# Kernel tuning notes

Hardware: AMD Instinct MI355X
Metric: run time of the kernel (lower is better)

Reference implementation:

```python
import jax, jax.numpy as jnp
import numpy as np

N = 100000   # num_nodes
E = 1600000  # num_edges
IN, HID, OUT = 128, 128, 64
BN_EPS = 1e-5


def setup_inputs() -> dict:
    key = jax.random.key(0)
    ks = jax.random.split(key, 8)
    x = jax.random.normal(ks[0], (N, IN), jnp.float32)
    edge_index = jax.random.randint(ks[1], (2, E), 0, N)
    edge_weight = jax.random.uniform(ks[2], (E,), jnp.float32)
    W1 = jax.random.normal(ks[3], (IN, HID), jnp.float32) / np.sqrt(IN)
    b1 = jnp.zeros((HID,), jnp.float32)
    gamma = jnp.ones((HID,), jnp.float32)
    beta = jnp.zeros((HID,), jnp.float32)
    W2 = jax.random.normal(ks[4], (HID, OUT), jnp.float32) / np.sqrt(HID)
    b2 = jnp.zeros((OUT,), jnp.float32)
    return {"x": x, "edge_index": edge_index, "edge_weight": edge_weight,
            "W1": W1, "b1": b1, "gamma": gamma, "beta": beta, "W2": W2, "b2": b2}


def _add_self_loops(edge_index, edge_weight, n):
    loops = jnp.arange(n, dtype=edge_index.dtype)
    row = jnp.concatenate([edge_index[0], loops])
    col = jnp.concatenate([edge_index[1], loops])
    ew = jnp.concatenate([edge_weight, jnp.ones((n,), edge_weight.dtype)])
    return row, col, ew


def _gcn_conv(x, row, col, ew, W, b, n):
    h = x @ W                                           # [n, out]
    deg = jax.ops.segment_sum(ew, col, num_segments=n)  # in-degree (incl. self-loops)
    dinv = jnp.where(deg > 0, jax.lax.rsqrt(jnp.where(deg > 0, deg, 1.0)), 0.0)
    norm = dinv[row] * ew * dinv[col]                   # [E+n]
    msg = h[row] * norm[:, None]                        # gather + scale
    out = jax.ops.segment_sum(msg, col, num_segments=n)  # scatter-add at targets
    return out + b


def reference(x, edge_index, edge_weight, W1, b1, gamma, beta, W2, b2):
    n = x.shape[0]
    row, col, ew = _add_self_loops(edge_index, edge_weight, n)
    h = _gcn_conv(x, row, col, ew, W1, b1, n)
    # BatchNorm1d over nodes (training-mode batch stats, biased variance)
    mu = h.mean(axis=0)
    var = ((h - mu) ** 2).mean(axis=0)
    h = (h - mu) * jax.lax.rsqrt(var + BN_EPS) * gamma + beta
    h = jax.nn.relu(h)
    # dropout is identity at inference
    h = _gcn_conv(h, row, col, ew, W2, b2, n)
    return jax.nn.log_softmax(h, axis=1)  # out_feats > 1 branch
```

## Files before the change

kernel.cpp:

```cpp
#include <hip/hip_runtime.h>
#include <math.h>


typedef unsigned int   uint;
typedef unsigned short ushort;
typedef __bf16 bf16x8 __attribute__((ext_vector_type(8)));
typedef float  f32x4  __attribute__((ext_vector_type(4)));

#define EPB  4096
#define BSH  9

union U16 { uint4 u; bf16x8 b; };

__device__ __forceinline__ void atomAddF(float* p, float v) {
    __hip_atomic_fetch_add(p, v, __ATOMIC_RELAXED, __HIP_MEMORY_SCOPE_AGENT);
}

__device__ __forceinline__ ushort f2bf(float f) {
    uint u = __float_as_uint(f);
    u += 0x7FFFu + ((u >> 16) & 1u);
    return (ushort)(u >> 16);
}
__device__ __forceinline__ float bf2f(ushort h) {
    return __uint_as_float(((uint)h) << 16);
}
__device__ __forceinline__ uint pack2(float f0, float f1) {
    return (uint)f2bf(f0) | ((uint)f2bf(f1) << 16);
}
__device__ __forceinline__ void fma8(float* acc, uint4 v, float w) {
    acc[0] = fmaf(bf2f((ushort)(v.x)),       w, acc[0]);
    acc[1] = fmaf(bf2f((ushort)(v.x >> 16)), w, acc[1]);
    acc[2] = fmaf(bf2f((ushort)(v.y)),       w, acc[2]);
    acc[3] = fmaf(bf2f((ushort)(v.y >> 16)), w, acc[3]);
    acc[4] = fmaf(bf2f((ushort)(v.z)),       w, acc[4]);
    acc[5] = fmaf(bf2f((ushort)(v.z >> 16)), w, acc[5]);
    acc[6] = fmaf(bf2f((ushort)(v.w)),       w, acc[6]);
    acc[7] = fmaf(bf2f((ushort)(v.w >> 16)), w, acc[7]);
}

__global__ __launch_bounds__(256)
void k_p1(const int* __restrict__ col, int* __restrict__ ghist,
          int e, int PB) {
    __shared__ int lh[256];
    lh[threadIdx.x] = 0;
    __syncthreads();
    int base = blockIdx.x * EPB;
    int end  = base + EPB; if (end > e) end = e;
    for (int j = base + threadIdx.x; j < end; j += 256)
        atomicAdd(&lh[col[j] >> BSH], 1);
    __syncthreads();
    ghist[threadIdx.x * PB + blockIdx.x] = lh[threadIdx.x];
}

__global__ __launch_bounds__(256)
void k_scanA(const int* __restrict__ v, int* __restrict__ bsum, int tot) {
    __shared__ int ls[256];
    int base = blockIdx.x * 1024 + threadIdx.x * 4;
    int s = 0;
#pragma unroll
    for (int k = 0; k < 4; ++k) { int i = base + k; if (i < tot) s += v[i]; }
    ls[threadIdx.x] = s;
    __syncthreads();
    for (int d = 128; d > 0; d >>= 1) {
        if (threadIdx.x < d) ls[threadIdx.x] += ls[threadIdx.x + d];
        __syncthreads();
    }
    if (threadIdx.x == 0) bsum[blockIdx.x] = ls[0];
}

__global__ __launch_bounds__(1024)
void k_scanB(int* __restrict__ bsum, float* __restrict__ bn, int nblk) {
    __shared__ int ls[1024];
    int t = threadIdx.x;
    if (t < 256) bn[t] = 0.0f;
    int v = (t < nblk) ? bsum[t] : 0;
    ls[t] = v;
    __syncthreads();
    for (int d = 1; d < 1024; d <<= 1) {
        int mine = ls[t];
        int up   = (t >= d) ? ls[t - d] : 0;
        __syncthreads();
        ls[t] = mine + up;
        __syncthreads();
    }
    if (t < nblk) bsum[t] = ls[t] - v;
}

__global__ __launch_bounds__(256)
void k_scanC(const int* __restrict__ v, const int* __restrict__ bsum,
             int* __restrict__ gout, int tot) {
    __shared__ int ls[256];
    int base = blockIdx.x * 1024 + threadIdx.x * 4;
    int w[4];
#pragma unroll
    for (int k = 0; k < 4; ++k) { int i = base + k; w[k] = (i < tot) ? v[i] : 0; }
    int t = w[0] + w[1] + w[2] + w[3];
    ls[threadIdx.x] = t;
    __syncthreads();
    for (int d = 1; d < 256; d <<= 1) {
        int mine = ls[threadIdx.x];
        int up   = (threadIdx.x >= d) ? ls[threadIdx.x - d] : 0;
        __syncthreads();
        ls[threadIdx.x] = mine + up;
        __syncthreads();
    }
    int off = bsum[blockIdx.x] + ls[threadIdx.x] - t;
    int pf = 0;
#pragma unroll
    for (int k = 0; k < 4; ++k) {
        int i = base + k;
        if (i < tot) gout[i] = off + pf;
        pf += w[k];
    }
}

__global__ __launch_bounds__(256)
void k_p3(const int* __restrict__ row, const int* __restrict__ col,
          const float* __restrict__ ew, const int* __restrict__ goff,
          int2* __restrict__ ebuf, int e, int PB) {
    __shared__ int cur[256];
    cur[threadIdx.x] = 0;
    __syncthreads();
    int blk  = blockIdx.x;
    int base = blk * EPB;
    int end  = base + EPB; if (end > e) end = e;
    for (int j = base + threadIdx.x; j < end; j += 256) {
        int c = col[j];
        int b = c >> BSH;
        int r = atomicAdd(&cur[b], 1);
        int pos = goff[b * PB + blk] + r;
        ebuf[pos] = make_int2(row[j] | ((c & ((1 << BSH) - 1)) << 17),
                              __float_as_int(ew[j]));
    }
}

__global__ __launch_bounds__(512)
void k_p4a(const int* __restrict__ goff, const int2* __restrict__ ebuf,
           int* __restrict__ ptr, float* __restrict__ dinv,
           int n, int e, int PB, int NB) {
    __shared__ int   cnt[512];
    __shared__ float fs[512];
    __shared__ int   sc[512];
    int tid = threadIdx.x;
    int b   = blockIdx.x;
    int bstart = goff[b * PB];
    int bend   = (b == NB - 1) ? e : goff[(b + 1) * PB];

    cnt[tid] = 0; fs[tid] = 0.f;
    __syncthreads();

    for (int j = bstart + tid; j < bend; j += 512) {
        int2 eb = ebuf[j];
        int c = (eb.x >> 17) & 511;
        atomicAdd(&cnt[c], 1);
        atomicAdd(&fs[c], __int_as_float(eb.y));
    }
    __syncthreads();

    int v = cnt[tid];
    sc[tid] = v;
    __syncthreads();
    for (int d = 1; d < 512; d <<= 1) {
        int mine = sc[tid];
        int up   = (tid >= d) ? sc[tid - d] : 0;
        __syncthreads();
        sc[tid] = mine + up;
        __syncthreads();
    }
    int excl = sc[tid] - v;

    int node = (b << BSH) + tid;
    if (node < n) {
        ptr[node]  = bstart + excl;
        dinv[node] = rsqrtf(1.0f + fs[tid]);
    }
    if (b == 0 && tid == 0) ptr[n] = e;
}

__global__ __launch_bounds__(512)
void k_p4b(const int* __restrict__ goff, const int2* __restrict__ ebuf,
           const int* __restrict__ ptr, const float* __restrict__ dinv,
           int2* __restrict__ csr, int n, int e, int PB, int NB) {
    __shared__ int   cur[512];
    __shared__ float dl[512];
    int tid = threadIdx.x;
    int b   = blockIdx.x;
    int bstart = goff[b * PB];
    int bend   = (b == NB - 1) ? e : goff[(b + 1) * PB];

    cur[tid] = 0;
    int node = (b << BSH) + tid;
    dl[tid] = (node < n) ? dinv[node] : 0.f;
    __syncthreads();

    for (int j = bstart + tid; j < bend; j += 512) {
        int2 eb = ebuf[j];
        int c   = (eb.x >> 17) & 511;
        int src = eb.x & 0x1FFFF;
        int r = atomicAdd(&cur[c], 1);
        float w = __int_as_float(eb.y) * dinv[src] * dl[c];
        csr[ptr[(b << BSH) + c] + r] = make_int2(src, __float_as_int(w));
    }
}

__global__ void k_wfrag(const float* __restrict__ W, uint4* __restrict__ Wf, int M) {
    int t = blockIdx.x * 256 + threadIdx.x;
    if (t >= M * 16) return;
    int l  = t & 63;
    int ks = (t >> 6) & 3;
    int nt = t >> 8;
    int kbase = ks * 32 + (l >> 4) * 8;
    int colj  = nt * 16 + (l & 15);
    float v[8];
#pragma unroll
    for (int j = 0; j < 8; ++j) v[j] = W[(kbase + j) * M + colj];
    uint4 o;
    o.x = pack2(v[0], v[1]);
    o.y = pack2(v[2], v[3]);
    o.z = pack2(v[4], v[5]);
    o.w = pack2(v[6], v[7]);
    Wf[t] = o;
}

template<int M, bool BN>
__global__ __launch_bounds__(256)
void k_mfma(const void* __restrict__ Xv, const uint4* __restrict__ Wf,
            const float* __restrict__ scale, const float* __restrict__ shift,
            ushort* __restrict__ H, int n)
{
    constexpr int NT = M / 16;
    const int l = threadIdx.x & 63;
    const int w = threadIdx.x >> 6;
    const int rowbase = blockIdx.x * 64 + w * 16;
    const int arow = rowbase + (l & 15);
    const bool rv = arow < n;
    const int koff = (l >> 4) * 8;

    f32x4 acc[NT];
#pragma unroll
    for (int t = 0; t < NT; ++t) acc[t] = (f32x4){0.f, 0.f, 0.f, 0.f};

#pragma unroll
    for (int ks = 0; ks < 4; ++ks) {
        U16 ua;
        if (BN) {
            const ushort* xr = (const ushort*)Xv + (size_t)arow * 128 + koff;
            U16 xa; xa.u = make_uint4(0, 0, 0, 0);
            if (rv) xa.u = *(const uint4*)(xr + ks * 32);
            int k0 = ks * 32 + koff;
            float4 sc0 = *(const float4*)(scale + k0);
            float4 sc1 = *(const float4*)(scale + k0 + 4);
            float4 sh0 = *(const float4*)(shift + k0);
            float4 sh1 = *(const float4*)(shift + k0 + 4);
            float a[8];
            a[0] = fmaxf(0.f, fmaf(bf2f((ushort)(xa.u.x)),       sc0.x, sh0.x));
            a[1] = fmaxf(0.f, fmaf(bf2f((ushort)(xa.u.x >> 16)), sc0.y, sh0.y));
            a[2] = fmaxf(0.f, fmaf(bf2f((ushort)(xa.u.y)),       sc0.z, sh0.z));
            a[3] = fmaxf(0.f, fmaf(bf2f((ushort)(xa.u.y >> 16)), sc0.w, sh0.w));
            a[4] = fmaxf(0.f, fmaf(bf2f((ushort)(xa.u.z)),       sc1.x, sh1.x));
            a[5] = fmaxf(0.f, fmaf(bf2f((ushort)(xa.u.z >> 16)), sc1.y, sh1.y));
            a[6] = fmaxf(0.f, fmaf(bf2f((ushort)(xa.u.w)),       sc1.z, sh1.z));
            a[7] = fmaxf(0.f, fmaf(bf2f((ushort)(xa.u.w >> 16)), sc1.w, sh1.w));
            ua.u.x = pack2(a[0], a[1]);
            ua.u.y = pack2(a[2], a[3]);
            ua.u.z = pack2(a[4], a[5]);
            ua.u.w = pack2(a[6], a[7]);
        } else {
            const float* xr = (const float*)Xv + (size_t)arow * 128 + koff;
            float4 a0 = make_float4(0.f, 0.f, 0.f, 0.f);
            float4 a1 = a0;
            if (rv) {
                a0 = *(const float4*)(xr + ks * 32);
                a1 = *(const float4*)(xr + ks * 32 + 4);
            }
            ua.u.x = pack2(a0.x, a0.y);
            ua.u.y = pack2(a0.z, a0.w);
            ua.u.z = pack2(a1.x, a1.y);
            ua.u.w = pack2(a1.z, a1.w);
        }
#pragma unroll
        for (int nt = 0; nt < NT; ++nt) {
            U16 ub;
            ub.u = Wf[(nt * 4 + ks) * 64 + l];
            acc[nt] = __builtin_amdgcn_mfma_f32_16x16x32_bf16(ua.b, ub.b, acc[nt], 0, 0, 0);
        }
    }

    __shared__ __align__(16) ushort lds[4][16][M + 8];
#pragma unroll
    for (int nt = 0; nt < NT; ++nt)
#pragma unroll
        for (int r = 0; r < 4; ++r)
            lds[w][(l >> 4) * 4 + r][nt * 16 + (l & 15)] = f2bf(acc[nt][r]);
    __syncthreads();

    constexpr int LPR = M / 8;
    constexpr int RPP = 64 / LPR;
#pragma unroll
    for (int it = 0; it < 16 / RPP; ++it) {
        int rl = it * RPP + (l / LPR);
        int gr = rowbase + rl;
        if (gr < n)
            *(uint4*)(H + (size_t)gr * M + (l % LPR) * 8) =
                *(const uint4*)&lds[w][rl][(l % LPR) * 8];
    }
}

__global__ __launch_bounds__(256)
void k_gather1(const int* __restrict__ ptr, const int2* __restrict__ csr,
               const ushort* __restrict__ h, const float* __restrict__ dinv,
               const float* __restrict__ bias, ushort* __restrict__ out, int n)
{
    int lane = threadIdx.x & 15;
    int node = (blockIdx.x * 256 + threadIdx.x) >> 4;
    if (node >= n) return;
    int p0 = ptr[node], p1 = ptr[node + 1];
    float di = dinv[node];
    float s  = di * di;

    U16 hv; hv.u = *(const uint4*)(h + (size_t)node * 128 + lane * 8);
    float acc[8];
    {
        const float* bp = bias + lane * 8;
#pragma unroll
        for (int k = 0; k < 8; ++k) acc[k] = bp[k];
        fma8(acc, hv.u, s);
    }

    int j = p0;
    int jend8 = p0 + ((p1 - p0) & ~7);
    for (; j < jend8; j += 8) {
        int2 pr[8];
#pragma unroll
        for (int k = 0; k < 8; ++k) pr[k] = csr[j + k];
        uint4 v[8];
#pragma unroll
        for (int k = 0; k < 8; ++k)
            v[k] = *(const uint4*)(h + (size_t)pr[k].x * 128 + lane * 8);
#pragma unroll
        for (int k = 0; k < 8; ++k)
            fma8(acc, v[k], __int_as_float(pr[k].y));
    }
    for (; j < p1; ++j) {
        int2 pr = csr[j];
        uint4 v = *(const uint4*)(h + (size_t)pr.x * 128 + lane * 8);
        fma8(acc, v, __int_as_float(pr.y));
    }

    U16 o;
    o.u.x = pack2(acc[0], acc[1]);
    o.u.y = pack2(acc[2], acc[3]);
    o.u.z = pack2(acc[4], acc[5]);
    o.u.w = pack2(acc[6], acc[7]);
    *(uint4*)(out + (size_t)node * 128 + lane * 8) = o.u;
}

__global__ __launch_bounds__(256)
void k_gather2(const int* __restrict__ ptr, const int2* __restrict__ csr,
               const ushort* __restrict__ h, const float* __restrict__ dinv,
               const float* __restrict__ bias, float* __restrict__ out, int n)
{
    int lane = threadIdx.x & 7;
    int node = (blockIdx.x * 256 + threadIdx.x) >> 3;
    if (node >= n) return;
    int p0 = ptr[node], p1 = ptr[node + 1];
    float di = dinv[node];
    float s  = di * di;

    U16 hv; hv.u = *(const uint4*)(h + (size_t)node * 64 + lane * 8);
    float acc[8];
    {
        const float* bp = bias + lane * 8;
#pragma unroll
        for (int k = 0; k < 8; ++k) acc[k] = bp[k];
        fma8(acc, hv.u, s);
    }

    int j = p0;
    int jend8 = p0 + ((p1 - p0) & ~7);
    for (; j < jend8; j += 8) {
        int2 pr[8];
#pragma unroll
        for (int k = 0; k < 8; ++k) pr[k] = csr[j + k];
        uint4 v[8];
#pragma unroll
        for (int k = 0; k < 8; ++k)
            v[k] = *(const uint4*)(h + (size_t)pr[k].x * 64 + lane * 8);
#pragma unroll
        for (int k = 0; k < 8; ++k)
            fma8(acc, v[k], __int_as_float(pr[k].y));
    }
    for (; j < p1; ++j) {
        int2 pr = csr[j];
        uint4 v = *(const uint4*)(h + (size_t)pr.x * 64 + lane * 8);
        fma8(acc, v, __int_as_float(pr.y));
    }

    float m = acc[0];
#pragma unroll
    for (int k = 1; k < 8; ++k) m = fmaxf(m, acc[k]);
#pragma unroll
    for (int off = 1; off < 8; off <<= 1) m = fmaxf(m, __shfl_xor(m, off, 64));
    float sum = 0.f;
#pragma unroll
    for (int k = 0; k < 8; ++k) sum += expf(acc[k] - m);
#pragma unroll
    for (int off = 1; off < 8; off <<= 1) sum += __shfl_xor(sum, off, 64);
    float lse = m + logf(sum);

    float* orow = out + (size_t)node * 64 + lane * 8;
    *(float4*)(orow)     = make_float4(acc[0] - lse, acc[1] - lse, acc[2] - lse, acc[3] - lse);
    *(float4*)(orow + 4) = make_float4(acc[4] - lse, acc[5] - lse, acc[6] - lse, acc[7] - lse);
}

__global__ __launch_bounds__(256)
void k_bn_stats(const ushort* __restrict__ a, float* __restrict__ sums,
                float* __restrict__ sumsq, int n)
{
    int fp = threadIdx.x & 63;
    int rg = threadIdx.x >> 6;
    float s0 = 0.f, q0 = 0.f, s1 = 0.f, q1 = 0.f;
    for (int r = blockIdx.x * 4 + rg; r < n; r += gridDim.x * 4) {
        uint v = *(const uint*)(a + (size_t)r * 128 + fp * 2);
        float x0 = bf2f((ushort)v), x1 = bf2f((ushort)(v >> 16));
        s0 += x0; q0 += x0 * x0;
        s1 += x1; q1 += x1 * x1;
    }
    __shared__ float l0[256], l1[256], l2[256], l3[256];
    l0[threadIdx.x] = s0; l1[threadIdx.x] = q0;
    l2[threadIdx.x] = s1; l3[threadIdx.x] = q1;
    __syncthreads();
    if (rg == 0) {
        float S0 = l0[fp] + l0[fp + 64] + l0[fp + 128] + l0[fp + 192];
        float Q0 = l1[fp] + l1[fp + 64] + l1[fp + 128] + l1[fp + 192];
        float S1 = l2[fp] + l2[fp + 64] + l2[fp + 128] + l2[fp + 192];
        float Q1 = l3[fp] + l3[fp + 64] + l3[fp + 128] + l3[fp + 192];
        atomAddF(&sums[fp * 2],      S0);
        atomAddF(&sumsq[fp * 2],     Q0);
        atomAddF(&sums[fp * 2 + 1],  S1);
        atomAddF(&sumsq[fp * 2 + 1], Q1);
    }
}

__global__ void k_bn_final(const float* __restrict__ bn, const float* __restrict__ gamma,
                           const float* __restrict__ beta, float* __restrict__ scale,
                           float* __restrict__ shift, int n)
{
    int f = threadIdx.x;
    if (f < 128) {
        float inv_n = 1.0f / (float)n;
        float mu  = bn[f] * inv_n;
        float var = bn[128 + f] * inv_n - mu * mu;
        float rstd = rsqrtf(var + 1e-5f);
        float sc = gamma[f] * rstd;
        scale[f] = sc;
        shift[f] = beta[f] - mu * sc;
    }
}

extern "C" void kernel_launch(void* const* d_in, const int* in_sizes, int n_in,
                              void* d_out, int out_size, void* d_ws, size_t ws_size,
                              hipStream_t stream)
{
    const float* x     = (const float*)d_in[0];
    const int*   ei    = (const int*)  d_in[1];
    const float* ew    = (const float*)d_in[2];
    const float* W1    = (const float*)d_in[3];
    const float* b1    = (const float*)d_in[4];
    const float* gamma = (const float*)d_in[5];
    const float* beta  = (const float*)d_in[6];
    const float* W2    = (const float*)d_in[7];
    const float* b2    = (const float*)d_in[8];

    const int n = in_sizes[0] / 128;
    const int e = in_sizes[2];
    const int* row = ei;
    const int* col = ei + e;

    const int PB  = (e + EPB - 1) / EPB;
    const int NB  = (n + (1 << BSH) - 1) >> BSH;
    const int tot = NB * PB;

    float* ws    = (float*)d_ws;
    size_t off   = 0;
    float* dinv  = ws + off; off += n;
    ushort* h1   = (ushort*)(ws + off); off += (size_t)n * 64;
    ushort* agg1 = (ushort*)(ws + off); off += (size_t)n * 64;
    float* bn    = ws + off; off += 256;
    float* scale = ws + off; off += 128;
    float* shift = ws + off; off += 128;
    int*   ptr   = (int*)(ws + off); off += (size_t)(n + 1);
    int*   bsum  = (int*)(ws + off); off += 1024;
    int*   ghist = (int*)(ws + off); off += (size_t)PB * 256;
    int*   goff  = (int*)(ws + off); off += (size_t)(tot + 1);
    off = (off + 3) & ~(size_t)3;
    uint4* w1f   = (uint4*)(ws + off); off += 8192;
    uint4* w2f   = (uint4*)(ws + off); off += 4096;
    int2*  ebuf  = (int2*)(ws + off); off += (size_t)e * 2;
    int2*  csr   = (int2*)(ws + off); off += (size_t)e * 2;
    ushort* h2   = h1;
    float* outp  = (float*)d_out;

    const int nb_qpn = (n + 15) / 16;
    const int nb_opn = (n + 31) / 32;
    const int nb_mf  = (n + 63) / 64;
    const int nblk_scan = (tot + 1023) / 1024;

    k_wfrag<<<8, 256, 0, stream>>>(W1, w1f, 128);
    k_wfrag<<<4, 256, 0, stream>>>(W2, w2f, 64);

    k_p1<<<PB, 256, 0, stream>>>(col, ghist, e, PB);
    k_scanA<<<nblk_scan, 256, 0, stream>>>(ghist, bsum, tot);
    k_scanB<<<1, 1024, 0, stream>>>(bsum, bn, nblk_scan);
    k_scanC<<<nblk_scan, 256, 0, stream>>>(ghist, bsum, goff, tot);
    k_p3<<<PB, 256, 0, stream>>>(row, col, ew, goff, ebuf, e, PB);
    k_p4a<<<NB, 512, 0, stream>>>(goff, ebuf, ptr, dinv, n, e, PB, NB);
    k_p4b<<<NB, 512, 0, stream>>>(goff, ebuf, ptr, dinv, csr, n, e, PB, NB);

    k_mfma<128, false><<<nb_mf, 256, 0, stream>>>(x, w1f, nullptr, nullptr, h1, n);
    k_gather1<<<nb_qpn, 256, 0, stream>>>(ptr, csr, h1, dinv, b1, agg1, n);

    k_bn_stats<<<256, 256, 0, stream>>>(agg1, bn, bn + 128, n);
    k_bn_final<<<1, 128, 0, stream>>>(bn, gamma, beta, scale, shift, n);

    k_mfma<64, true><<<nb_mf, 256, 0, stream>>>(agg1, w2f, scale, shift, h2, n);
    k_gather2<<<nb_opn, 256, 0, stream>>>(ptr, csr, h2, dinv, b2, outp, n);
}
```

Baseline: 256.8 us.

## Fuse CSR build passes, defer edge normalization to gather, merge small kernels

The two CSR-building passes (degree/prefix and scatter) become one kernel. It keeps per-node offsets in shared memory and writes raw edge weights into the CSR, so the separate pass that re-read ebuf and gathered dinv[src] goes away. Both gather kernels now compute the symmetric normalization on the fly with an extra dinv[src] load per edge. The BN finalize kernel is folded into the second MFMA kernel's prologue, the two weight-fragment kernels become one launch, and edges per partition block are doubled. The trade-off is fewer launches and fewer passes over the edge buffer in exchange for extra random dinv loads in both gathers and redundant BN-finalize work in every block.

```diff
diff --git a/kernel.cpp b/kernel.cpp
--- a/kernel.cpp
+++ b/kernel.cpp
@@ -7,7 +7,7 @@
 typedef __bf16 bf16x8 __attribute__((ext_vector_type(8)));
 typedef float  f32x4  __attribute__((ext_vector_type(4)));
 
-#define EPB  4096
+#define EPB  8192
 #define BSH  9
 
 union U16 { uint4 u; bf16x8 b; };
@@ -135,18 +135,19 @@
 }
 
 __global__ __launch_bounds__(512)
-void k_p4a(const int* __restrict__ goff, const int2* __restrict__ ebuf,
-           int* __restrict__ ptr, float* __restrict__ dinv,
-           int n, int e, int PB, int NB) {
+void k_p4(const int* __restrict__ goff, const int2* __restrict__ ebuf,
+          int2* __restrict__ csr, int* __restrict__ ptr,
+          float* __restrict__ dinv, int n, int e, int PB, int NB) {
     __shared__ int   cnt[512];
     __shared__ float fs[512];
+    __shared__ int   cur2[512];
     __shared__ int   sc[512];
     int tid = threadIdx.x;
     int b   = blockIdx.x;
     int bstart = goff[b * PB];
     int bend   = (b == NB - 1) ? e : goff[(b + 1) * PB];
 
-    cnt[tid] = 0; fs[tid] = 0.f;
+    cnt[tid] = 0; fs[tid] = 0.f; cur2[tid] = 0;
     __syncthreads();
 
     for (int j = bstart + tid; j < bend; j += 512) {
@@ -174,38 +175,20 @@
         ptr[node]  = bstart + excl;
         dinv[node] = rsqrtf(1.0f + fs[tid]);
     }
-    if (b == 0 && tid == 0) ptr[n] = e;
-}
-
-__global__ __launch_bounds__(512)
-void k_p4b(const int* __restrict__ goff, const int2* __restrict__ ebuf,
-           const int* __restrict__ ptr, const float* __restrict__ dinv,
-           int2* __restrict__ csr, int n, int e, int PB, int NB) {
-    __shared__ int   cur[512];
-    __shared__ float dl[512];
-    int tid = threadIdx.x;
-    int b   = blockIdx.x;
-    int bstart = goff[b * PB];
-    int bend   = (b == NB - 1) ? e : goff[(b + 1) * PB];
-
-    cur[tid] = 0;
-    int node = (b << BSH) + tid;
-    dl[tid] = (node < n) ? dinv[node] : 0.f;
+    cnt[tid] = excl;
     __syncthreads();
 
     for (int j = bstart + tid; j < bend; j += 512) {
         int2 eb = ebuf[j];
-        int c   = (eb.x >> 17) & 511;
-        int src = eb.x & 0x1FFFF;
-        int r = atomicAdd(&cur[c], 1);
-        float w = __int_as_float(eb.y) * dinv[src] * dl[c];
-        csr[ptr[(b << BSH) + c] + r] = make_int2(src, __float_as_int(w));
-    }
-}
-
-__global__ void k_wfrag(const float* __restrict__ W, uint4* __restrict__ Wf, int M) {
-    int t = blockIdx.x * 256 + threadIdx.x;
-    if (t >= M * 16) return;
+        int c = (eb.x >> 17) & 511;
+        int r = atomicAdd(&cur2[c], 1);
+        csr[bstart + cnt[c] + r] = make_int2(eb.x & 0x1FFFF, eb.y);
+    }
+    if (b == 0 && tid == 0) ptr[n] = e;
+}
+
+__device__ __forceinline__ void wfrag_one(const float* __restrict__ W,
+                                          uint4* __restrict__ Wf, int M, int t) {
     int l  = t & 63;
     int ks = (t >> 6) & 3;
     int nt = t >> 8;
@@ -222,11 +205,18 @@
     Wf[t] = o;
 }
 
+__global__ void k_wfrag(const float* __restrict__ W1, const float* __restrict__ W2,
+                        uint4* __restrict__ w1f, uint4* __restrict__ w2f) {
+    int t = blockIdx.x * 256 + threadIdx.x;
+    if (t < 2048)      wfrag_one(W1, w1f, 128, t);
+    else if (t < 3072) wfrag_one(W2, w2f, 64, t - 2048);
+}
+
 template<int M, bool BN>
 __global__ __launch_bounds__(256)
 void k_mfma(const void* __restrict__ Xv, const uint4* __restrict__ Wf,
-            const float* __restrict__ scale, const float* __restrict__ shift,
-            ushort* __restrict__ H, int n)
+            const float* __restrict__ bnsum, const float* __restrict__ gamma,
+            const float* __restrict__ beta, ushort* __restrict__ H, int n)
 {
     constexpr int NT = M / 16;
     const int l = threadIdx.x & 63;
@@ -236,6 +226,22 @@
     const bool rv = arow < n;
     const int koff = (l >> 4) * 8;
 
+    __shared__ float sc_s[BN ? 128 : 1];
+    __shared__ float sh_s[BN ? 128 : 1];
+    if (BN) {
+        int f = threadIdx.x;
+        if (f < 128) {
+            float inv_n = 1.0f / (float)n;
+            float mu  = bnsum[f] * inv_n;
+            float var = bnsum[128 + f] * inv_n - mu * mu;
+            float rstd = rsqrtf(var + 1e-5f);
+            float sc = gamma[f] * rstd;
+            sc_s[f] = sc;
+            sh_s[f] = beta[f] - mu * sc;
+        }
+        __syncthreads();
+    }
+
     f32x4 acc[NT];
 #pragma unroll
     for (int t = 0; t < NT; ++t) acc[t] = (f32x4){0.f, 0.f, 0.f, 0.f};
@@ -248,19 +254,15 @@
             U16 xa; xa.u = make_uint4(0, 0, 0, 0);
             if (rv) xa.u = *(const uint4*)(xr + ks * 32);
             int k0 = ks * 32 + koff;
-            float4 sc0 = *(const float4*)(scale + k0);
-            float4 sc1 = *(const float4*)(scale + k0 + 4);
-            float4 sh0 = *(const float4*)(shift + k0);
-            float4 sh1 = *(const float4*)(shift + k0 + 4);
             float a[8];
-            a[0] = fmaxf(0.f, fmaf(bf2f((ushort)(xa.u.x)),       sc0.x, sh0.x));
-            a[1] = fmaxf(0.f, fmaf(bf2f((ushort)(xa.u.x >> 16)), sc0.y, sh0.y));
-            a[2] = fmaxf(0.f, fmaf(bf2f((ushort)(xa.u.y)),       sc0.z, sh0.z));
-            a[3] = fmaxf(0.f, fmaf(bf2f((ushort)(xa.u.y >> 16)), sc0.w, sh0.w));
-            a[4] = fmaxf(0.f, fmaf(bf2f((ushort)(xa.u.z)),       sc1.x, sh1.x));
-            a[5] = fmaxf(0.f, fmaf(bf2f((ushort)(xa.u.z >> 16)), sc1.y, sh1.y));
-            a[6] = fmaxf(0.f, fmaf(bf2f((ushort)(xa.u.w)),       sc1.z, sh1.z));
-            a[7] = fmaxf(0.f, fmaf(bf2f((ushort)(xa.u.w >> 16)), sc1.w, sh1.w));
+            a[0] = fmaxf(0.f, fmaf(bf2f((ushort)(xa.u.x)),       sc_s[k0+0], sh_s[k0+0]));
+            a[1] = fmaxf(0.f, fmaf(bf2f((ushort)(xa.u.x >> 16)), sc_s[k0+1], sh_s[k0+1]));
+            a[2] = fmaxf(0.f, fmaf(bf2f((ushort)(xa.u.y)),       sc_s[k0+2], sh_s[k0+2]));
+            a[3] = fmaxf(0.f, fmaf(bf2f((ushort)(xa.u.y >> 16)), sc_s[k0+3], sh_s[k0+3]));
+            a[4] = fmaxf(0.f, fmaf(bf2f((ushort)(xa.u.z)),       sc_s[k0+4], sh_s[k0+4]));
+            a[5] = fmaxf(0.f, fmaf(bf2f((ushort)(xa.u.z >> 16)), sc_s[k0+5], sh_s[k0+5]));
+            a[6] = fmaxf(0.f, fmaf(bf2f((ushort)(xa.u.w)),       sc_s[k0+6], sh_s[k0+6]));
+            a[7] = fmaxf(0.f, fmaf(bf2f((ushort)(xa.u.w >> 16)), sc_s[k0+7], sh_s[k0+7]));
             ua.u.x = pack2(a[0], a[1]);
             ua.u.y = pack2(a[2], a[3]);
             ua.u.z = pack2(a[4], a[5]);
@@ -333,18 +335,21 @@
         int2 pr[8];
 #pragma unroll
         for (int k = 0; k < 8; ++k) pr[k] = csr[j + k];
+        float dv[8];
+#pragma unroll
+        for (int k = 0; k < 8; ++k) dv[k] = dinv[pr[k].x];
         uint4 v[8];
 #pragma unroll
         for (int k = 0; k < 8; ++k)
             v[k] = *(const uint4*)(h + (size_t)pr[k].x * 128 + lane * 8);
 #pragma unroll
         for (int k = 0; k < 8; ++k)
-            fma8(acc, v[k], __int_as_float(pr[k].y));
+            fma8(acc, v[k], __int_as_float(pr[k].y) * di * dv[k]);
     }
     for (; j < p1; ++j) {
         int2 pr = csr[j];
         uint4 v = *(const uint4*)(h + (size_t)pr.x * 128 + lane * 8);
-        fma8(acc, v, __int_as_float(pr.y));
+        fma8(acc, v, __int_as_float(pr.y) * di * dinv[pr.x]);
     }
 
     U16 o;
@@ -382,18 +387,21 @@
         int2 pr[8];
 #pragma unroll
         for (int k = 0; k < 8; ++k) pr[k] = csr[j + k];
+        float dv[8];
+#pragma unroll
+        for (int k = 0; k < 8; ++k) dv[k] = dinv[pr[k].x];
         uint4 v[8];
 #pragma unroll
         for (int k = 0; k < 8; ++k)
             v[k] = *(const uint4*)(h + (size_t)pr[k].x * 64 + lane * 8);
 #pragma unroll
         for (int k = 0; k < 8; ++k)
-            fma8(acc, v[k], __int_as_float(pr[k].y));
+            fma8(acc, v[k], __int_as_float(pr[k].y) * di * dv[k]);
     }
     for (; j < p1; ++j) {
         int2 pr = csr[j];
         uint4 v = *(const uint4*)(h + (size_t)pr.x * 64 + lane * 8);
-        fma8(acc, v, __int_as_float(pr.y));
+        fma8(acc, v, __int_as_float(pr.y) * di * dinv[pr.x]);
     }
 
     float m = acc[0];
@@ -439,22 +447,6 @@
         atomAddF(&sumsq[fp * 2],     Q0);
         atomAddF(&sums[fp * 2 + 1],  S1);
         atomAddF(&sumsq[fp * 2 + 1], Q1);
-    }
-}
-
-__global__ void k_bn_final(const float* __restrict__ bn, const float* __restrict__ gamma,
-                           const float* __restrict__ beta, float* __restrict__ scale,
-                           float* __restrict__ shift, int n)
-{
-    int f = threadIdx.x;
-    if (f < 128) {
-        float inv_n = 1.0f / (float)n;
-        float mu  = bn[f] * inv_n;
-        float var = bn[128 + f] * inv_n - mu * mu;
-        float rstd = rsqrtf(var + 1e-5f);
-        float sc = gamma[f] * rstd;
-        scale[f] = sc;
-        shift[f] = beta[f] - mu * sc;
     }
 }
 
@@ -487,8 +479,6 @@
     ushort* h1   = (ushort*)(ws + off); off += (size_t)n * 64;
     ushort* agg1 = (ushort*)(ws + off); off += (size_t)n * 64;
     float* bn    = ws + off; off += 256;
-    float* scale = ws + off; off += 128;
-    float* shift = ws + off; off += 128;
     int*   ptr   = (int*)(ws + off); off += (size_t)(n + 1);
     int*   bsum  = (int*)(ws + off); off += 1024;
     int*   ghist = (int*)(ws + off); off += (size_t)PB * 256;
@@ -506,23 +496,20 @@
     const int nb_mf  = (n + 63) / 64;
     const int nblk_scan = (tot + 1023) / 1024;
 
-    k_wfrag<<<8, 256, 0, stream>>>(W1, w1f, 128);
-    k_wfrag<<<4, 256, 0, stream>>>(W2, w2f, 64);
+    k_wfrag<<<12, 256, 0, stream>>>(W1, W2, w1f, w2f);
 
     k_p1<<<PB, 256, 0, stream>>>(col, ghist, e, PB);
     k_scanA<<<nblk_scan, 256, 0, stream>>>(ghist, bsum, tot);
     k_scanB<<<1, 1024, 0, stream>>>(bsum, bn, nblk_scan);
     k_scanC<<<nblk_scan, 256, 0, stream>>>(ghist, bsum, goff, tot);
     k_p3<<<PB, 256, 0, stream>>>(row, col, ew, goff, ebuf, e, PB);
-    k_p4a<<<NB, 512, 0, stream>>>(goff, ebuf, ptr, dinv, n, e, PB, NB);
-    k_p4b<<<NB, 512, 0, stream>>>(goff, ebuf, ptr, dinv, csr, n, e, PB, NB);
-
-    k_mfma<128, false><<<nb_mf, 256, 0, stream>>>(x, w1f, nullptr, nullptr, h1, n);
+    k_p4<<<NB, 512, 0, stream>>>(goff, ebuf, csr, ptr, dinv, n, e, PB, NB);
+
+    k_mfma<128, false><<<nb_mf, 256, 0, stream>>>(x, w1f, nullptr, nullptr, nullptr, h1, n);
     k_gather1<<<nb_qpn, 256, 0, stream>>>(ptr, csr, h1, dinv, b1, agg1, n);
 
     k_bn_stats<<<256, 256, 0, stream>>>(agg1, bn, bn + 128, n);
-    k_bn_final<<<1, 128, 0, stream>>>(bn, gamma, beta, scale, shift, n);
-
-    k_mfma<64, true><<<nb_mf, 256, 0, stream>>>(agg1, w2f, scale, shift, h2, n);
+
+    k_mfma<64, true><<<nb_mf, 256, 0, stream>>>(agg1, w2f, bn, gamma, beta, h2, n);
     k_gather2<<<nb_opn, 256, 0, stream>>>(ptr, csr, h2, dinv, b2, outp, n);
 }
```

After: 255.9 us. About the same (-0.3%).
